# Optimization experiments

Measured on AMD Instinct MI355X. Metric: run time of the kernel, lower is better.

The kernel has to match this reference:

```python
import jax, jax.numpy as jnp
import numpy as np

B, S, D = 4, 1024, 1024
H = 16
HD = D // H  # 64
NPOS = 64


def setup_inputs() -> dict:
    key = jax.random.key(0)
    ks = jax.random.split(key, 12)
    f = lambda k, shape, s=0.02: jax.random.normal(k, shape, dtype=jnp.float32) * s
    return {
        "q": jax.random.normal(ks[0], (B, S, D), dtype=jnp.float32),
        "k": jax.random.normal(ks[1], (B, S, D), dtype=jnp.float32),
        "v": jax.random.normal(ks[2], (B, S, D), dtype=jnp.float32),
        "Wq_w": f(ks[3], (D, D)), "Wq_b": f(ks[4], (D,)),
        "Wk_w": f(ks[5], (D, D)), "Wk_b": f(ks[6], (D,)),
        "Wv_w": f(ks[7], (D, D)), "Wv_b": f(ks[8], (D,)),
        "Wo_w": f(ks[9], (D, D)), "Wo_b": f(ks[10], (D,)),
        "pos_emb": f(ks[11], (HD, NPOS)),  # torch param is [1,1,head_dim,npos_max]
    }


def _proj(x, w, b):
    # nn.Linear: x @ w.T + b, then split heads -> [B, H, S, HD]
    y = jnp.einsum("bsd,ed->bse", x, w) + b
    bsz, s, _ = y.shape
    return y.reshape(bsz, s, H, HD).transpose(0, 2, 1, 3)


def reference(q, k, v, Wq_w, Wq_b, Wk_w, Wk_b, Wv_w, Wv_b, Wo_w, Wo_b, pos_emb):
    Q = _proj(q, Wq_w, Wq_b)
    K = _proj(k, Wk_w, Wk_b)
    V = _proj(v, Wv_w, Wv_b)

    scale = 1.0 / np.sqrt(HD).astype(np.float32)
    logits = jnp.einsum("bhqd,bhkd->bhqk", Q, K) * scale  # [B,H,S,S]

    # CoPE: sigmoid gates -> reverse cumsum -> interpolated position-logit gather
    gates = jax.nn.sigmoid(logits)
    pos = jnp.flip(jnp.cumsum(jnp.flip(gates, axis=-1), axis=-1), axis=-1)
    pos = jnp.minimum(pos, NPOS - 1)
    pos_floor = jnp.floor(pos)
    pos_ceil = jnp.ceil(pos)
    logits_int = jnp.einsum("bhqd,dn->bhqn", Q, pos_emb)  # [B,H,S,NPOS]
    lc = jnp.take_along_axis(logits_int, pos_ceil.astype(jnp.int32), axis=-1)
    lf = jnp.take_along_axis(logits_int, pos_floor.astype(jnp.int32), axis=-1)
    w = pos - pos_floor
    logits = logits + lc * w + lf * (1.0 - w)

    score = jax.nn.softmax(logits, axis=-1)
    out = jnp.einsum("bhqk,bhkd->bhqd", score, V)
    out = out.transpose(0, 2, 1, 3).reshape(q.shape[0], q.shape[1], D)
    return jnp.einsum("bsd,ed->bse", out, Wo_w) + Wo_b
```

## Files before the change

### kernel.cpp

```cpp
#include <hip/hip_runtime.h>
#include <hip/hip_bf16.h>

typedef __attribute__((ext_vector_type(8))) short short8;
typedef __attribute__((ext_vector_type(4))) float f32x4;
typedef unsigned short us;

#define MFMA16(a,b,c) __builtin_amdgcn_mfma_f32_16x16x32_bf16((a),(b),(c),0,0,0)
#define LOG2E 1.4426950408889634f

static __device__ __forceinline__ us bf16r(float x){
  unsigned u = __builtin_bit_cast(unsigned, x);
  u = u + 0x7fffu + ((u >> 16) & 1u);
  return (us)(u >> 16);
}
static __device__ __forceinline__ unsigned pk2(float a, float b){
  return (unsigned)bf16r(a) | ((unsigned)bf16r(b) << 16);
}
static __device__ __forceinline__ short8 cvt8(float4 a, float4 b){
  uint4 u; u.x = pk2(a.x, a.y); u.y = pk2(a.z, a.w);
  u.z = pk2(b.x, b.y); u.w = pk2(b.z, b.w);
  return __builtin_bit_cast(short8, u);
}
static __device__ __forceinline__ float b2f(us h){
  return __builtin_bit_cast(float, (unsigned)h << 16);
}
static __device__ __forceinline__ float exp2fast(float x){
  float r; asm("v_exp_f32 %0, %1" : "=v"(r) : "v"(x)); return r;
}
static __device__ __forceinline__ float rcpfast(float x){
  float r; asm("v_rcp_f32 %0, %1" : "=v"(r) : "v"(x)); return r;
}

__global__ __launch_bounds__(256)
void transpose_pe(const float* __restrict__ pe, us* __restrict__ peT){
  const int t = threadIdx.x;
  const int n = t & 63, dq = t >> 6;
#pragma unroll
  for (int j = 0; j < 16; ++j){
    const int d = dq * 16 + j;
    peT[n * 64 + d] = bf16r(pe[d * 64 + n] * LOG2E);
  }
}

__global__ __launch_bounds__(256)
void transpose_v(const us* __restrict__ Vb, us* __restrict__ VT){
  __shared__ __align__(16) us tile[64 * 72];
  const int t = threadIdx.x;
  const int stile = blockIdx.x & 15;
  const int bh = blockIdx.x >> 4;
  const int b = bh >> 4, h = bh & 15;
  const int s0 = stile << 6;
#pragma unroll
  for (int c = 0; c < 2; ++c){
    const int idx = t + (c << 8);
    const int sr = idx >> 3, cw = idx & 7;
    *(short8*)&tile[sr * 72 + cw * 8] =
        *(const short8*)(Vb + ((size_t)(b * 1024 + s0 + sr)) * 1024 + h * 64 + cw * 8);
  }
  __syncthreads();
#pragma unroll
  for (int c = 0; c < 2; ++c){
    const int idx = t + (c << 8);
    const int dr = idx >> 3, sw = idx & 7;
    short8 o;
#pragma unroll
    for (int j = 0; j < 8; ++j) o[j] = (short)tile[(sw * 8 + j) * 72 + dr];
    *(short8*)(VT + ((size_t)(bh * 64 + dr)) * 1024 + s0 + sw * 8) = o;
  }
}

template<bool A_BF16, bool OUT_BF16>
__global__ __launch_bounds__(256)
void gemm3(const void* __restrict__ Av0, const void* __restrict__ Av1, const void* __restrict__ Av2,
           const float* __restrict__ W0, const float* __restrict__ W1, const float* __restrict__ W2,
           const float* __restrict__ bp0, const float* __restrict__ bp1, const float* __restrict__ bp2,
           void* __restrict__ O0, void* __restrict__ O1, void* __restrict__ O2){
  __shared__ __align__(16) us Al[128 * 64];
  __shared__ __align__(16) us Bl[128 * 64];
  const int sel = blockIdx.y;
  const void* Av   = sel == 0 ? Av0 : (sel == 1 ? Av1 : Av2);
  const float* Wm  = sel == 0 ? W0  : (sel == 1 ? W1  : W2);
  const float* bias = sel == 0 ? bp0 : (sel == 1 ? bp1 : bp2);
  void* Ov         = sel == 0 ? O0  : (sel == 1 ? O1  : O2);
  const int tid = threadIdx.x;
  const int bm = blockIdx.x & 31, bn = blockIdx.x >> 5;
  const int m0 = bm << 7, n0 = bn << 7;
  const int w = tid >> 6, l = tid & 63;
  const int lr = l & 15, lg = l >> 4;
  const int wm = (w & 1) << 6, wn = (w >> 1) << 6;
  int srow[4], scol[4], sdst[4];
#pragma unroll
  for (int c = 0; c < 4; ++c){
    const int idx = tid + (c << 8);
    const int r = idx >> 3, cw = idx & 7;
    srow[c] = r; scol[c] = cw << 3;
    sdst[c] = r * 64 + ((cw << 3) ^ ((r & 7) << 3));
  }
  const int swz = (lr & 7) << 3;
  f32x4 acc[4][4];
#pragma unroll
  for (int i = 0; i < 4; ++i)
#pragma unroll
    for (int j = 0; j < 4; ++j) acc[i][j] = (f32x4){0.f, 0.f, 0.f, 0.f};

  auto ldA = [&](int c, int k) -> short8 {
    if constexpr (A_BF16){
      return *(const short8*)((const us*)Av + (size_t)(m0 + srow[c]) * 1024 + k + scol[c]);
    } else {
      const float* p = (const float*)Av + (size_t)(m0 + srow[c]) * 1024 + k + scol[c];
      return cvt8(*(const float4*)p, *(const float4*)(p + 4));
    }
  };
  auto ldW = [&](int c, int k) -> short8 {
    const float* p = Wm + (size_t)(n0 + srow[c]) * 1024 + k + scol[c];
    return cvt8(*(const float4*)p, *(const float4*)(p + 4));
  };

  short8 av[4], bv[4];
#pragma unroll
  for (int c = 0; c < 4; ++c){ av[c] = ldA(c, 0); bv[c] = ldW(c, 0); }

  for (int k0 = 0; k0 < 1024; k0 += 64){
    __syncthreads();
#pragma unroll
    for (int c = 0; c < 4; ++c){
      *(short8*)&Al[sdst[c]] = av[c];
      *(short8*)&Bl[sdst[c]] = bv[c];
    }
    __syncthreads();
    if (k0 < 960){
#pragma unroll
      for (int c = 0; c < 4; ++c){ av[c] = ldA(c, k0 + 64); bv[c] = ldW(c, k0 + 64); }
    }
#pragma unroll
    for (int ks = 0; ks < 2; ++ks){
      short8 af[4], bfv[4];
#pragma unroll
      for (int mt = 0; mt < 4; ++mt)
        af[mt] = *(const short8*)&Al[(wm + mt * 16 + lr) * 64 + (((ks << 5) + (lg << 3)) ^ swz)];
#pragma unroll
      for (int nt = 0; nt < 4; ++nt)
        bfv[nt] = *(const short8*)&Bl[(wn + nt * 16 + lr) * 64 + (((ks << 5) + (lg << 3)) ^ swz)];
#pragma unroll
      for (int mt = 0; mt < 4; ++mt)
#pragma unroll
        for (int nt = 0; nt < 4; ++nt)
          acc[mt][nt] = MFMA16(af[mt], bfv[nt], acc[mt][nt]);
    }
  }
  float bb[4];
#pragma unroll
  for (int nt = 0; nt < 4; ++nt) bb[nt] = bias[n0 + wn + nt * 16 + lr];
#pragma unroll
  for (int mt = 0; mt < 4; ++mt)
#pragma unroll
    for (int nt = 0; nt < 4; ++nt)
#pragma unroll
      for (int r = 0; r < 4; ++r){
        const size_t m = m0 + wm + mt * 16 + lg * 4 + r;
        const size_t n = n0 + wn + nt * 16 + lr;
        const float vv = acc[mt][nt][r] + bb[nt];
        if (OUT_BF16) ((us*)Ov)[m * 1024 + n] = bf16r(vv);
        else          ((float*)Ov)[m * 1024 + n] = vv;
      }
}

__global__ __launch_bounds__(256, 4)
void cope_attn_v3(const us* __restrict__ Qb, const us* __restrict__ Kb,
                  const us* __restrict__ VT, const us* __restrict__ peT,
                  us* __restrict__ Ob){
  __shared__ __align__(16) us yl[16 * 1024];
  __shared__ float li2[16][68];
  const int tid = threadIdx.x;
  const int w = tid >> 6, l = tid & 63;
  const int lr = l & 15, lg = l >> 4;
  const int qt = blockIdx.x & 63;
  const int bh = blockIdx.x >> 6;
  const int b = bh >> 4, h = bh & 15;
  const int q0 = qt << 4;
  const us* Qh = Qb + ((size_t)(b * 1024 + q0)) * 1024 + h * 64;
  const us* Kh = Kb + ((size_t)(b * 1024)) * 1024 + h * 64;
  const us* Vh = VT + ((size_t)bh) * 64 * 1024;
  const float QSC = 0.125f * LOG2E;

  const short8 aq0 = *(const short8*)(Qh + (size_t)lr * 1024 + lg * 8);
  const short8 aq1 = *(const short8*)(Qh + (size_t)lr * 1024 + 32 + lg * 8);

  {
    f32x4 a = (f32x4){0.f, 0.f, 0.f, 0.f};
    const short8 p0 = *(const short8*)(peT + (size_t)(w * 16 + lr) * 64 + lg * 8);
    const short8 p1 = *(const short8*)(peT + (size_t)(w * 16 + lr) * 64 + 32 + lg * 8);
    a = MFMA16(aq0, p0, a);
    a = MFMA16(aq1, p1, a);
#pragma unroll
    for (int r = 0; r < 4; ++r) li2[lg * 4 + r][w * 16 + lr] = a[r];
  }
  {
    const int kbase = w << 8;
    const us* Kw = Kh + (size_t)(kbase + lr) * 1024 + lg * 8;
    short8 b0 = *(const short8*)(Kw);
    short8 b1 = *(const short8*)(Kw + 32);
    for (int t = 0; t < 16; ++t){
      short8 n0v = b0, n1v = b1;
      if (t < 15){
        const us* Kn = Kw + (size_t)((t + 1) * 16) * 1024;
        n0v = *(const short8*)(Kn);
        n1v = *(const short8*)(Kn + 32);
      }
      f32x4 a = (f32x4){0.f, 0.f, 0.f, 0.f};
      a = MFMA16(aq0, b0, a);
      a = MFMA16(aq1, b1, a);
#pragma unroll
      for (int r = 0; r < 4; ++r){
        const int row = lg * 4 + r;
        const int kc = kbase + t * 16 + lr;
        yl[row * 1024 + (((kc >> 3) ^ (row & 7)) << 3) + (kc & 7)] = bf16r(a[r] * QSC);
      }
      b0 = n0v; b1 = n1v;
    }
  }
  __syncthreads();
#pragma unroll
  for (int rr = 0; rr < 4; ++rr){
    const int row = w * 4 + rr;
    const int sz = row & 7;
    const int ad0 = row * 1024 + (((2 * l) ^ sz) << 3);
    const int ad1 = row * 1024 + (((2 * l + 1) ^ sz) << 3);
    const short8 y0 = *(const short8*)&yl[ad0];
    const short8 y1 = *(const short8*)&yl[ad1];
    float x[16];
#pragma unroll
    for (int j = 0; j < 8; ++j){ x[j] = b2f((us)y0[j]); x[8 + j] = b2f((us)y1[j]); }
    float pref[16];
    float s = 0.f;
#pragma unroll
    for (int i = 0; i < 16; ++i){
      const float g = rcpfast(1.f + exp2fast(-x[i]));
      pref[i] = s;
      s += g;
    }
    float run = s;
#pragma unroll
    for (int off = 1; off < 64; off <<= 1){
      const float t2 = __shfl_up(run, off);
      if (l >= off) run += t2;
    }
    const float T = __shfl(run, 63);
    const float base = T - (run - s);
    float mx = -3.4e38f;
#pragma unroll
    for (int i = 0; i < 16; ++i){
      float p = base - pref[i];
      p = fminf(p, 63.f);
      p = fmaxf(p, 0.f);
      const float pf = floorf(p);
      const int il = (int)pf;
      const int ic = (int)ceilf(p);
      const float wt = p - pf;
      const float xx = x[i] + li2[row][ic] * wt + li2[row][il] * (1.f - wt);
      x[i] = xx;
      mx = fmaxf(mx, xx);
    }
#pragma unroll
    for (int off = 1; off < 64; off <<= 1) mx = fmaxf(mx, __shfl_xor(mx, off));
    float sum = 0.f;
#pragma unroll
    for (int i = 0; i < 16; ++i){ const float e = exp2fast(x[i] - mx); x[i] = e; sum += e; }
#pragma unroll
    for (int off = 1; off < 64; off <<= 1) sum += __shfl_xor(sum, off);
    const float inv = rcpfast(sum);
    uint4 ua, ub;
    ua.x = pk2(x[0] * inv,  x[1] * inv);  ua.y = pk2(x[2] * inv,  x[3] * inv);
    ua.z = pk2(x[4] * inv,  x[5] * inv);  ua.w = pk2(x[6] * inv,  x[7] * inv);
    ub.x = pk2(x[8] * inv,  x[9] * inv);  ub.y = pk2(x[10] * inv, x[11] * inv);
    ub.z = pk2(x[12] * inv, x[13] * inv); ub.w = pk2(x[14] * inv, x[15] * inv);
    *(uint4*)&yl[ad0] = ua;
    *(uint4*)&yl[ad1] = ub;
  }
  __syncthreads();
  {
    const int d0 = w * 16;
    const int psw = lr & 7;
    f32x4 a = (f32x4){0.f, 0.f, 0.f, 0.f};
    const us* Vw = Vh + (size_t)(d0 + lr) * 1024 + lg * 8;
    short8 vb = *(const short8*)(Vw);
    for (int ks = 0; ks < 32; ++ks){
      short8 vn = vb;
      if (ks < 31) vn = *(const short8*)(Vw + (ks + 1) * 32);
      const short8 pa = *(const short8*)&yl[lr * 1024 + ((((ks << 2) + lg) ^ psw) << 3)];
      a = MFMA16(pa, vb, a);
      vb = vn;
    }
#pragma unroll
    for (int r = 0; r < 4; ++r)
      Ob[((size_t)(b * 1024 + q0 + lg * 4 + r)) * 1024 + h * 64 + d0 + lr] = bf16r(a[r]);
  }
}

extern "C" void kernel_launch(void* const* d_in, const int* in_sizes, int n_in,
                              void* d_out, int out_size, void* d_ws, size_t ws_size,
                              hipStream_t stream) {
  const float* q    = (const float*)d_in[0];
  const float* k    = (const float*)d_in[1];
  const float* v    = (const float*)d_in[2];
  const float* Wq_w = (const float*)d_in[3];
  const float* Wq_b = (const float*)d_in[4];
  const float* Wk_w = (const float*)d_in[5];
  const float* Wk_b = (const float*)d_in[6];
  const float* Wv_w = (const float*)d_in[7];
  const float* Wv_b = (const float*)d_in[8];
  const float* Wo_w = (const float*)d_in[9];
  const float* Wo_b = (const float*)d_in[10];
  const float* pe   = (const float*)d_in[11];
  float* out = (float*)d_out;

  char* W = (char*)d_ws;
  const size_t MB = (size_t)1 << 20;
  us* Qbf = (us*)(W);
  us* Kbf = (us*)(W + 8 * MB);
  us* Vbf = (us*)(W + 16 * MB);
  us* VTb = (us*)(W + 24 * MB);
  us* Obf = (us*)(W + 32 * MB);
  us* peT = (us*)(W + 40 * MB);

  transpose_pe<<<1, 256, 0, stream>>>(pe, peT);
  gemm3<false, true><<<dim3(256, 3), 256, 0, stream>>>(
      q, k, v, Wq_w, Wk_w, Wv_w, Wq_b, Wk_b, Wv_b, Qbf, Kbf, Vbf);
  transpose_v<<<1024, 256, 0, stream>>>(Vbf, VTb);
  cope_attn_v3<<<4096, 256, 0, stream>>>(Qbf, Kbf, VTb, peT, Obf);
  gemm3<true, false><<<dim3(256, 1), 256, 0, stream>>>(
      Obf, Obf, Obf, Wo_w, Wo_w, Wo_w, Wo_b, Wo_b, Wo_b, out, out, out);
}
```

Before: 220.5 us.

## Use 512-thread blocks in CoPE attention with split-K PV reduction and saturated-position fast path

Doubles the attention block to 8 waves, so each wave computes half as many QK key tiles and softmax rows. The PV product is split across two wave groups along the key dimension, with partial sums reduced through shared memory. A fast path skips the interpolated gather when every position in a lane's chunk is saturated at 63, and the ceil index becomes floor+1. This adds an extra barrier and reuses li2 as scratch, and raises the occupancy target, which may pressure registers.

```diff
diff --git a/kernel.cpp b/kernel.cpp
--- a/kernel.cpp
+++ b/kernel.cpp
@@ -165,8 +165,8 @@
       }
 }
 
-__global__ __launch_bounds__(256, 4)
-void cope_attn_v3(const us* __restrict__ Qb, const us* __restrict__ Kb,
+__global__ __launch_bounds__(512, 8)
+void cope_attn_v4(const us* __restrict__ Qb, const us* __restrict__ Kb,
                   const us* __restrict__ VT, const us* __restrict__ peT,
                   us* __restrict__ Ob){
   __shared__ __align__(16) us yl[16 * 1024];
@@ -186,7 +186,7 @@
   const short8 aq0 = *(const short8*)(Qh + (size_t)lr * 1024 + lg * 8);
   const short8 aq1 = *(const short8*)(Qh + (size_t)lr * 1024 + 32 + lg * 8);
 
-  {
+  if (w < 4){
     f32x4 a = (f32x4){0.f, 0.f, 0.f, 0.f};
     const short8 p0 = *(const short8*)(peT + (size_t)(w * 16 + lr) * 64 + lg * 8);
     const short8 p1 = *(const short8*)(peT + (size_t)(w * 16 + lr) * 64 + 32 + lg * 8);
@@ -196,13 +196,13 @@
     for (int r = 0; r < 4; ++r) li2[lg * 4 + r][w * 16 + lr] = a[r];
   }
   {
-    const int kbase = w << 8;
+    const int kbase = w << 7;
     const us* Kw = Kh + (size_t)(kbase + lr) * 1024 + lg * 8;
     short8 b0 = *(const short8*)(Kw);
     short8 b1 = *(const short8*)(Kw + 32);
-    for (int t = 0; t < 16; ++t){
+    for (int t = 0; t < 8; ++t){
       short8 n0v = b0, n1v = b1;
-      if (t < 15){
+      if (t < 7){
         const us* Kn = Kw + (size_t)((t + 1) * 16) * 1024;
         n0v = *(const short8*)(Kn);
         n1v = *(const short8*)(Kn + 32);
@@ -221,8 +221,8 @@
   }
   __syncthreads();
 #pragma unroll
-  for (int rr = 0; rr < 4; ++rr){
-    const int row = w * 4 + rr;
+  for (int rr = 0; rr < 2; ++rr){
+    const int row = w * 2 + rr;
     const int sz = row & 7;
     const int ad0 = row * 1024 + (((2 * l) ^ sz) << 3);
     const int ad1 = row * 1024 + (((2 * l + 1) ^ sz) << 3);
@@ -247,19 +247,29 @@
     }
     const float T = __shfl(run, 63);
     const float base = T - (run - s);
+    const float li63 = li2[row][63];
     float mx = -3.4e38f;
-#pragma unroll
-    for (int i = 0; i < 16; ++i){
-      float p = base - pref[i];
-      p = fminf(p, 63.f);
-      p = fmaxf(p, 0.f);
-      const float pf = floorf(p);
-      const int il = (int)pf;
-      const int ic = (int)ceilf(p);
-      const float wt = p - pf;
-      const float xx = x[i] + li2[row][ic] * wt + li2[row][il] * (1.f - wt);
-      x[i] = xx;
-      mx = fmaxf(mx, xx);
+    if (base - pref[15] >= 63.f){
+#pragma unroll
+      for (int i = 0; i < 16; ++i){
+        const float xx = x[i] + li63;
+        x[i] = xx;
+        mx = fmaxf(mx, xx);
+      }
+    } else {
+#pragma unroll
+      for (int i = 0; i < 16; ++i){
+        float p = base - pref[i];
+        p = fminf(p, 63.f);
+        p = fmaxf(p, 0.f);
+        const float pf = floorf(p);
+        const int il = (int)pf;
+        const int ic = min(il + 1, 63);
+        const float wt = p - pf;
+        const float xx = x[i] + li2[row][ic] * wt + li2[row][il] * (1.f - wt);
+        x[i] = xx;
+        mx = fmaxf(mx, xx);
+      }
     }
 #pragma unroll
     for (int off = 1; off < 64; off <<= 1) mx = fmaxf(mx, __shfl_xor(mx, off));
@@ -279,21 +289,32 @@
   }
   __syncthreads();
   {
-    const int d0 = w * 16;
+    const int d0 = (w & 3) << 4;
+    const int kh = w >> 2;
     const int psw = lr & 7;
     f32x4 a = (f32x4){0.f, 0.f, 0.f, 0.f};
-    const us* Vw = Vh + (size_t)(d0 + lr) * 1024 + lg * 8;
+    const us* Vw = Vh + (size_t)(d0 + lr) * 1024 + (kh << 9) + lg * 8;
     short8 vb = *(const short8*)(Vw);
-    for (int ks = 0; ks < 32; ++ks){
+    for (int ks = 0; ks < 16; ++ks){
       short8 vn = vb;
-      if (ks < 31) vn = *(const short8*)(Vw + (ks + 1) * 32);
-      const short8 pa = *(const short8*)&yl[lr * 1024 + ((((ks << 2) + lg) ^ psw) << 3)];
+      if (ks < 15) vn = *(const short8*)(Vw + (ks + 1) * 32);
+      const int kstep = kh * 16 + ks;
+      const short8 pa = *(const short8*)&yl[lr * 1024 + ((((kstep << 2) + lg) ^ psw) << 3)];
       a = MFMA16(pa, vb, a);
       vb = vn;
     }
-#pragma unroll
-    for (int r = 0; r < 4; ++r)
-      Ob[((size_t)(b * 1024 + q0 + lg * 4 + r)) * 1024 + h * 64 + d0 + lr] = bf16r(a[r]);
+    if (w >= 4){
+#pragma unroll
+      for (int r = 0; r < 4; ++r) li2[lg * 4 + r][d0 + lr] = a[r];
+    }
+    __syncthreads();
+    if (w < 4){
+#pragma unroll
+      for (int r = 0; r < 4; ++r){
+        const float val = a[r] + li2[lg * 4 + r][d0 + lr];
+        Ob[((size_t)(b * 1024 + q0 + lg * 4 + r)) * 1024 + h * 64 + d0 + lr] = bf16r(val);
+      }
+    }
   }
 }
 
@@ -327,7 +348,7 @@
   gemm3<false, true><<<dim3(256, 3), 256, 0, stream>>>(
       q, k, v, Wq_w, Wk_w, Wv_w, Wq_b, Wk_b, Wv_b, Qbf, Kbf, Vbf);
   transpose_v<<<1024, 256, 0, stream>>>(Vbf, VTb);
-  cope_attn_v3<<<4096, 256, 0, stream>>>(Qbf, Kbf, VTb, peT, Obf);
+  cope_attn_v4<<<4096, 512, 0, stream>>>(Qbf, Kbf, VTb, peT, Obf);
   gemm3<true, false><<<dim3(256, 1), 256, 0, stream>>>(
       Obf, Obf, Obf, Wo_w, Wo_w, Wo_w, Wo_b, Wo_b, Wo_b, out, out, out);
 }
```

Result: slower. 230.5 us (+4.5%).

## Halve query tile to 8 rows, pack position logits, drop softmax max pass

Applied to the files above, without the earlier changes.

The attention kernel now handles 8 query rows per block instead of 16, which halves shared memory and doubles the grid with higher launch-bound occupancy. Half of each MFMA tile is duplicated rows whose results are discarded. Position logits are stored as packed bf16 floor/ceil pairs, so a single 32-bit LDS read serves the interpolation. The softmax max-reduction is removed and exp is taken directly, relying on bounded logits; this adds a risk of overflow, while bf16 position logits lose some precision. Block IDs are remapped to interleave across XCDs, and each K/V read now feeds half as many useful query rows.

```diff
diff --git a/kernel.cpp b/kernel.cpp
--- a/kernel.cpp
+++ b/kernel.cpp
@@ -165,26 +165,28 @@
       }
 }
 
-__global__ __launch_bounds__(256, 4)
-void cope_attn_v3(const us* __restrict__ Qb, const us* __restrict__ Kb,
+__global__ __launch_bounds__(256, 8)
+void cope_attn_v5(const us* __restrict__ Qb, const us* __restrict__ Kb,
                   const us* __restrict__ VT, const us* __restrict__ peT,
                   us* __restrict__ Ob){
-  __shared__ __align__(16) us yl[16 * 1024];
-  __shared__ float li2[16][68];
+  __shared__ __align__(16) us yl[8 * 1024];
+  __shared__ __align__(4) us pkt[8 * 128];
   const int tid = threadIdx.x;
   const int w = tid >> 6, l = tid & 63;
   const int lr = l & 15, lg = l >> 4;
-  const int qt = blockIdx.x & 63;
-  const int bh = blockIdx.x >> 6;
+  const int wgid = (blockIdx.x & 7) * 1024 + (blockIdx.x >> 3);
+  const int qt = wgid & 127;
+  const int bh = wgid >> 7;
   const int b = bh >> 4, h = bh & 15;
-  const int q0 = qt << 4;
+  const int q0 = qt << 3;
   const us* Qh = Qb + ((size_t)(b * 1024 + q0)) * 1024 + h * 64;
   const us* Kh = Kb + ((size_t)(b * 1024)) * 1024 + h * 64;
   const us* Vh = VT + ((size_t)bh) * 64 * 1024;
   const float QSC = 0.125f * LOG2E;
 
-  const short8 aq0 = *(const short8*)(Qh + (size_t)lr * 1024 + lg * 8);
-  const short8 aq1 = *(const short8*)(Qh + (size_t)lr * 1024 + 32 + lg * 8);
+  const int qrow = lr & 7;
+  const short8 aq0 = *(const short8*)(Qh + (size_t)qrow * 1024 + lg * 8);
+  const short8 aq1 = *(const short8*)(Qh + (size_t)qrow * 1024 + 32 + lg * 8);
 
   {
     f32x4 a = (f32x4){0.f, 0.f, 0.f, 0.f};
@@ -192,8 +194,17 @@
     const short8 p1 = *(const short8*)(peT + (size_t)(w * 16 + lr) * 64 + 32 + lg * 8);
     a = MFMA16(aq0, p0, a);
     a = MFMA16(aq1, p1, a);
-#pragma unroll
-    for (int r = 0; r < 4; ++r) li2[lg * 4 + r][w * 16 + lr] = a[r];
+    if (lg < 2){
+      const int n = w * 16 + lr;
+#pragma unroll
+      for (int r = 0; r < 4; ++r){
+        const int row = lg * 4 + r;
+        const us v = bf16r(a[r]);
+        pkt[row * 128 + 2 * n] = v;
+        if (n > 0)  pkt[row * 128 + 2 * n - 1] = v;
+        if (n == 63) pkt[row * 128 + 127] = v;
+      }
+    }
   }
   {
     const int kbase = w << 8;
@@ -210,22 +221,24 @@
       f32x4 a = (f32x4){0.f, 0.f, 0.f, 0.f};
       a = MFMA16(aq0, b0, a);
       a = MFMA16(aq1, b1, a);
-#pragma unroll
-      for (int r = 0; r < 4; ++r){
-        const int row = lg * 4 + r;
+      if (lg < 2){
         const int kc = kbase + t * 16 + lr;
-        yl[row * 1024 + (((kc >> 3) ^ (row & 7)) << 3) + (kc & 7)] = bf16r(a[r] * QSC);
+#pragma unroll
+        for (int r = 0; r < 4; ++r){
+          const int row = lg * 4 + r;
+          yl[row * 1024 + (((kc >> 3) ^ row) << 3) + (kc & 7)] = bf16r(a[r] * QSC);
+        }
       }
       b0 = n0v; b1 = n1v;
     }
   }
   __syncthreads();
-#pragma unroll
-  for (int rr = 0; rr < 4; ++rr){
-    const int row = w * 4 + rr;
-    const int sz = row & 7;
-    const int ad0 = row * 1024 + (((2 * l) ^ sz) << 3);
-    const int ad1 = row * 1024 + (((2 * l + 1) ^ sz) << 3);
+  const unsigned* upk = (const unsigned*)pkt;
+#pragma unroll
+  for (int rr = 0; rr < 2; ++rr){
+    const int row = w * 2 + rr;
+    const int ad0 = row * 1024 + (((2 * l) ^ row) << 3);
+    const int ad1 = row * 1024 + (((2 * l + 1) ^ row) << 3);
     const short8 y0 = *(const short8*)&yl[ad0];
     const short8 y1 = *(const short8*)&yl[ad1];
     float x[16];
@@ -247,7 +260,7 @@
     }
     const float T = __shfl(run, 63);
     const float base = T - (run - s);
-    float mx = -3.4e38f;
+    float sum = 0.f;
 #pragma unroll
     for (int i = 0; i < 16; ++i){
       float p = base - pref[i];
@@ -255,17 +268,14 @@
       p = fmaxf(p, 0.f);
       const float pf = floorf(p);
       const int il = (int)pf;
-      const int ic = (int)ceilf(p);
       const float wt = p - pf;
-      const float xx = x[i] + li2[row][ic] * wt + li2[row][il] * (1.f - wt);
-      x[i] = xx;
-      mx = fmaxf(mx, xx);
-    }
-#pragma unroll
-    for (int off = 1; off < 64; off <<= 1) mx = fmaxf(mx, __shfl_xor(mx, off));
-    float sum = 0.f;
-#pragma unroll
-    for (int i = 0; i < 16; ++i){ const float e = exp2fast(x[i] - mx); x[i] = e; sum += e; }
+      const unsigned pr = upk[row * 64 + il];
+      const float lo = __builtin_bit_cast(float, pr << 16);
+      const float hi = __builtin_bit_cast(float, pr & 0xffff0000u);
+      const float e = exp2fast(x[i] + lo + wt * (hi - lo));
+      x[i] = e;
+      sum += e;
+    }
 #pragma unroll
     for (int off = 1; off < 64; off <<= 1) sum += __shfl_xor(sum, off);
     const float inv = rcpfast(sum);
@@ -287,13 +297,15 @@
     for (int ks = 0; ks < 32; ++ks){
       short8 vn = vb;
       if (ks < 31) vn = *(const short8*)(Vw + (ks + 1) * 32);
-      const short8 pa = *(const short8*)&yl[lr * 1024 + ((((ks << 2) + lg) ^ psw) << 3)];
+      const short8 pa = *(const short8*)&yl[(lr & 7) * 1024 + ((((ks << 2) + lg) ^ psw) << 3)];
       a = MFMA16(pa, vb, a);
       vb = vn;
     }
-#pragma unroll
-    for (int r = 0; r < 4; ++r)
-      Ob[((size_t)(b * 1024 + q0 + lg * 4 + r)) * 1024 + h * 64 + d0 + lr] = bf16r(a[r]);
+    if (lg < 2){
+#pragma unroll
+      for (int r = 0; r < 4; ++r)
+        Ob[((size_t)(b * 1024 + q0 + lg * 4 + r)) * 1024 + h * 64 + d0 + lr] = bf16r(a[r]);
+    }
   }
 }
 
@@ -327,7 +339,7 @@
   gemm3<false, true><<<dim3(256, 3), 256, 0, stream>>>(
       q, k, v, Wq_w, Wk_w, Wv_w, Wq_b, Wk_b, Wv_b, Qbf, Kbf, Vbf);
   transpose_v<<<1024, 256, 0, stream>>>(Vbf, VTb);
-  cope_attn_v3<<<4096, 256, 0, stream>>>(Qbf, Kbf, VTb, peT, Obf);
+  cope_attn_v5<<<8192, 256, 0, stream>>>(Qbf, Kbf, VTb, peT, Obf);
   gemm3<true, false><<<dim3(256, 1), 256, 0, stream>>>(
       Obf, Obf, Obf, Wo_w, Wo_w, Wo_w, Wo_b, Wo_b, Wo_b, out, out, out);
 }
```

New measurement: 337.3 us. +53.0%, slower.

## Use bpermute lerp table and drop softmax max pass in CoPE attention

Applied to the files above, without the earlier changes.

Position logits are stored in registers as packed (value, next-difference) bf16 pairs. The interpolated gather is now a ds_bpermute plus one FMA, replacing two LDS reads with floor/ceil. The softmax max reduction is removed, and exp2 runs directly on the logits. Float-to-bf16 packing uses the hardware v_cvt_pk_bf16_f32 instruction, and the occupancy hint is raised to 5. This cuts VALU, LDS and shuffle work, but it risks overflow when logits are large and lowers the precision of the position-logit table.

```diff
diff --git a/kernel.cpp b/kernel.cpp
--- a/kernel.cpp
+++ b/kernel.cpp
@@ -13,12 +13,12 @@
   u = u + 0x7fffu + ((u >> 16) & 1u);
   return (us)(u >> 16);
 }
-static __device__ __forceinline__ unsigned pk2(float a, float b){
-  return (unsigned)bf16r(a) | ((unsigned)bf16r(b) << 16);
+static __device__ __forceinline__ unsigned cvtpk(float a, float b){
+  unsigned r; asm("v_cvt_pk_bf16_f32 %0, %1, %2" : "=v"(r) : "v"(a), "v"(b)); return r;
 }
 static __device__ __forceinline__ short8 cvt8(float4 a, float4 b){
-  uint4 u; u.x = pk2(a.x, a.y); u.y = pk2(a.z, a.w);
-  u.z = pk2(b.x, b.y); u.w = pk2(b.z, b.w);
+  uint4 u; u.x = cvtpk(a.x, a.y); u.y = cvtpk(a.z, a.w);
+  u.z = cvtpk(b.x, b.y); u.w = cvtpk(b.z, b.w);
   return __builtin_bit_cast(short8, u);
 }
 static __device__ __forceinline__ float b2f(us h){
@@ -29,6 +29,9 @@
 }
 static __device__ __forceinline__ float rcpfast(float x){
   float r; asm("v_rcp_f32 %0, %1" : "=v"(r) : "v"(x)); return r;
+}
+static __device__ __forceinline__ float fractfast(float x){
+  float r; asm("v_fract_f32 %0, %1" : "=v"(r) : "v"(x)); return r;
 }
 
 __global__ __launch_bounds__(256)
@@ -165,12 +168,11 @@
       }
 }
 
-__global__ __launch_bounds__(256, 4)
-void cope_attn_v3(const us* __restrict__ Qb, const us* __restrict__ Kb,
+__global__ __launch_bounds__(256, 5)
+void cope_attn_v6(const us* __restrict__ Qb, const us* __restrict__ Kb,
                   const us* __restrict__ VT, const us* __restrict__ peT,
                   us* __restrict__ Ob){
   __shared__ __align__(16) us yl[16 * 1024];
-  __shared__ float li2[16][68];
   const int tid = threadIdx.x;
   const int w = tid >> 6, l = tid & 63;
   const int lr = l & 15, lg = l >> 4;
@@ -193,8 +195,19 @@
     a = MFMA16(aq0, p0, a);
     a = MFMA16(aq1, p1, a);
 #pragma unroll
-    for (int r = 0; r < 4; ++r) li2[lg * 4 + r][w * 16 + lr] = a[r];
-  }
+    for (int r = 0; r < 4; ++r) yl[(lg * 4 + r) * 64 + w * 16 + lr] = bf16r(a[r]);
+  }
+  __syncthreads();
+  unsigned trow[4];
+#pragma unroll
+  for (int rr = 0; rr < 4; ++rr){
+    const int row = w * 4 + rr;
+    const us lov = yl[row * 64 + l];
+    const us hiv = (l < 63) ? yl[row * 64 + l + 1] : lov;
+    const float dif = b2f(hiv) - b2f(lov);
+    trow[rr] = (unsigned)lov | ((unsigned)bf16r(dif) << 16);
+  }
+  __syncthreads();
   {
     const int kbase = w << 8;
     const us* Kw = Kh + (size_t)(kbase + lr) * 1024 + lg * 8;
@@ -210,12 +223,14 @@
       f32x4 a = (f32x4){0.f, 0.f, 0.f, 0.f};
       a = MFMA16(aq0, b0, a);
       a = MFMA16(aq1, b1, a);
-#pragma unroll
-      for (int r = 0; r < 4; ++r){
-        const int row = lg * 4 + r;
-        const int kc = kbase + t * 16 + lr;
-        yl[row * 1024 + (((kc >> 3) ^ (row & 7)) << 3) + (kc & 7)] = bf16r(a[r] * QSC);
-      }
+      const int kc = kbase + t * 16 + lr;
+      const unsigned p01 = cvtpk(a[0] * QSC, a[1] * QSC);
+      const unsigned p23 = cvtpk(a[2] * QSC, a[3] * QSC);
+      const int r0 = lg * 4;
+      yl[(r0 + 0) * 1024 + (((kc >> 3) ^ ((r0 + 0) & 7)) << 3) + (kc & 7)] = (us)p01;
+      yl[(r0 + 1) * 1024 + (((kc >> 3) ^ ((r0 + 1) & 7)) << 3) + (kc & 7)] = (us)(p01 >> 16);
+      yl[(r0 + 2) * 1024 + (((kc >> 3) ^ ((r0 + 2) & 7)) << 3) + (kc & 7)] = (us)p23;
+      yl[(r0 + 3) * 1024 + (((kc >> 3) ^ ((r0 + 3) & 7)) << 3) + (kc & 7)] = (us)(p23 >> 16);
       b0 = n0v; b1 = n1v;
     }
   }
@@ -247,33 +262,29 @@
     }
     const float T = __shfl(run, 63);
     const float base = T - (run - s);
-    float mx = -3.4e38f;
+    const unsigned tbl = trow[rr];
+    float sum = 0.f;
 #pragma unroll
     for (int i = 0; i < 16; ++i){
       float p = base - pref[i];
-      p = fminf(p, 63.f);
-      p = fmaxf(p, 0.f);
-      const float pf = floorf(p);
-      const int il = (int)pf;
-      const int ic = (int)ceilf(p);
-      const float wt = p - pf;
-      const float xx = x[i] + li2[row][ic] * wt + li2[row][il] * (1.f - wt);
-      x[i] = xx;
-      mx = fmaxf(mx, xx);
-    }
-#pragma unroll
-    for (int off = 1; off < 64; off <<= 1) mx = fmaxf(mx, __shfl_xor(mx, off));
-    float sum = 0.f;
-#pragma unroll
-    for (int i = 0; i < 16; ++i){ const float e = exp2fast(x[i] - mx); x[i] = e; sum += e; }
+      p = __builtin_amdgcn_fmed3f(p, 0.f, 63.f);
+      const int il = (int)p;
+      const float wt = fractfast(p);
+      const unsigned pr = (unsigned)__builtin_amdgcn_ds_bpermute(il << 2, (int)tbl);
+      const float lo  = __builtin_bit_cast(float, pr << 16);
+      const float dif = __builtin_bit_cast(float, pr & 0xffff0000u);
+      const float e = exp2fast(x[i] + lo + wt * dif);
+      x[i] = e;
+      sum += e;
+    }
 #pragma unroll
     for (int off = 1; off < 64; off <<= 1) sum += __shfl_xor(sum, off);
     const float inv = rcpfast(sum);
     uint4 ua, ub;
-    ua.x = pk2(x[0] * inv,  x[1] * inv);  ua.y = pk2(x[2] * inv,  x[3] * inv);
-    ua.z = pk2(x[4] * inv,  x[5] * inv);  ua.w = pk2(x[6] * inv,  x[7] * inv);
-    ub.x = pk2(x[8] * inv,  x[9] * inv);  ub.y = pk2(x[10] * inv, x[11] * inv);
-    ub.z = pk2(x[12] * inv, x[13] * inv); ub.w = pk2(x[14] * inv, x[15] * inv);
+    ua.x = cvtpk(x[0] * inv,  x[1] * inv);  ua.y = cvtpk(x[2] * inv,  x[3] * inv);
+    ua.z = cvtpk(x[4] * inv,  x[5] * inv);  ua.w = cvtpk(x[6] * inv,  x[7] * inv);
+    ub.x = cvtpk(x[8] * inv,  x[9] * inv);  ub.y = cvtpk(x[10] * inv, x[11] * inv);
+    ub.z = cvtpk(x[12] * inv, x[13] * inv); ub.w = cvtpk(x[14] * inv, x[15] * inv);
     *(uint4*)&yl[ad0] = ua;
     *(uint4*)&yl[ad1] = ub;
   }
@@ -327,7 +338,7 @@
   gemm3<false, true><<<dim3(256, 3), 256, 0, stream>>>(
       q, k, v, Wq_w, Wk_w, Wv_w, Wq_b, Wk_b, Wv_b, Qbf, Kbf, Vbf);
   transpose_v<<<1024, 256, 0, stream>>>(Vbf, VTb);
-  cope_attn_v3<<<4096, 256, 0, stream>>>(Qbf, Kbf, VTb, peT, Obf);
+  cope_attn_v6<<<4096, 256, 0, stream>>>(Qbf, Kbf, VTb, peT, Obf);
   gemm3<true, false><<<dim3(256, 1), 256, 0, stream>>>(
       Obf, Obf, Obf, Wo_w, Wo_w, Wo_w, Wo_b, Wo_b, Wo_b, out, out, out);
 }
```

New measurement: 221.1 us. Within noise of the previous version (+0.3%).
